# Kernel tuning notes

Measured on AMD Instinct MI355X. Metric: run time of the kernel, lower is better.

The kernel has to match this reference:

```python
import jax, jax.numpy as jnp
import numpy as np

N = 100000      # nodes
E = 1200000     # edges
F = 16          # in_cont_dim
EMB = 8         # emb_dim
H = 64          # hidden_dim
NL = 3          # num_layers
NT = 32         # num_func_types


def setup_inputs() -> dict:
    key = jax.random.key(0)
    ks = jax.random.split(key, 10)
    s = lambda k, sh: jax.random.normal(k, sh, jnp.float32) * 0.05
    inp = {}
    inp["x_cont"] = jax.random.normal(ks[0], (N, F), jnp.float32)
    inp["func_type"] = jax.random.randint(ks[1], (N,), 0, NT)
    inp["edge_index"] = jax.random.randint(ks[2], (2, E), 0, N)
    inp["emb_table"] = s(ks[3], (NT, EMB))
    inp["W_in"] = s(ks[4], (F + EMB, H)); inp["b_in"] = jnp.zeros((H,), jnp.float32)
    inp["W_g"] = s(ks[5], (NL, H, H));    inp["b_g"] = jnp.zeros((NL, H), jnp.float32)
    inp["W_o1"] = s(ks[6], (H, H));       inp["b_o1"] = jnp.zeros((H,), jnp.float32)
    inp["W_o2"] = s(ks[7], (H, 1));       inp["b_o2"] = jnp.zeros((1,), jnp.float32)
    return inp


def _gcn_layer(x, src, dst, deg_isq, W, b):
    # PyG GCNConv: h = x W; out_i = sum_{j->i} d_i^-1/2 d_j^-1/2 h_j + d_i^-1 h_i + b
    h = x @ W                                   # [N, H]
    norm = deg_isq[src] * deg_isq[dst]          # [E]
    agg = jax.ops.segment_sum(norm[:, None] * h[src], dst, num_segments=N)
    agg = agg + (deg_isq * deg_isq)[:, None] * h  # self-loop contribution
    return agg + b


def reference(x_cont, func_type, edge_index, emb_table, W_in, b_in,
              W_g, b_g, W_o1, b_o1, W_o2, b_o2):
    src, dst = edge_index[0], edge_index[1]
    # degree with self loops (weight 1), computed at target nodes as in gcn_norm
    deg = 1.0 + jax.ops.segment_sum(jnp.ones((E,), x_cont.dtype), dst, num_segments=N)
    deg_isq = jax.lax.rsqrt(deg)
    x = jnp.concatenate([x_cont, emb_table[func_type]], axis=-1)  # [N, F+EMB]
    x = jax.nn.relu(x @ W_in + b_in)
    for i in range(NL):
        x = jax.nn.relu(_gcn_layer(x, src, dst, deg_isq, W_g[i], b_g[i]))
        # dropout is identity in eval mode
    h = jax.nn.relu(x @ W_o1 + b_o1)
    return (h @ W_o2 + b_o2)[:, 0]  # [N]
```

## Files before the change

### kernel.cpp

```cpp
#include <hip/hip_runtime.h>

#define HD 64
#define FC 16
#define FEMB 8

__device__ __forceinline__ float bfu(unsigned u) { return __uint_as_float(u); }
__device__ __forceinline__ unsigned short f2bf(float f) {
    unsigned u = __float_as_uint(f);
    return (unsigned short)((u + 0x7fffu + ((u >> 16) & 1u)) >> 16);
}

__global__ void k_count_rank(const int* __restrict__ dst, int* __restrict__ cnt,
                             int* __restrict__ rank, int E) {
    int t = blockIdx.x * blockDim.x + threadIdx.x;
    int base = t * 4;
    if (base + 4 <= E) {
        int4 d = *(const int4*)(dst + base);
        int r0 = atomicAdd(&cnt[d.x], 1);
        int r1 = atomicAdd(&cnt[d.y], 1);
        int r2 = atomicAdd(&cnt[d.z], 1);
        int r3 = atomicAdd(&cnt[d.w], 1);
        *(int4*)(rank + base) = make_int4(r0, r1, r2, r3);
    } else {
        for (int e = base; e < E; e++)
            rank[e] = atomicAdd(&cnt[dst[e]], 1);
    }
}

__global__ void k_scan1(const int* __restrict__ cnt, int* __restrict__ row_part,
                        int* __restrict__ bsum, float* __restrict__ disq, int n) {
    __shared__ int s[256];
    int t = threadIdx.x;
    int i = blockIdx.x * 256 + t;
    int v = (i < n) ? cnt[i] : 0;
    if (i < n) disq[i] = rsqrtf(1.0f + (float)v);
    s[t] = v;
    __syncthreads();
    for (int off = 1; off < 256; off <<= 1) {
        int a = (t >= off) ? s[t - off] : 0;
        __syncthreads();
        s[t] += a;
        __syncthreads();
    }
    if (i < n) row_part[i] = s[t] - v;
    if (t == 255) bsum[blockIdx.x] = s[255];
}

__global__ void k_scan2(int* __restrict__ bsum, int nb) {
    __shared__ int s[1024];
    int t = threadIdx.x;
    int v = (t < nb) ? bsum[t] : 0;
    s[t] = v;
    __syncthreads();
    for (int off = 1; off < 1024; off <<= 1) {
        int a = (t >= off) ? s[t - off] : 0;
        __syncthreads();
        s[t] += a;
        __syncthreads();
    }
    if (t < nb) bsum[t] = s[t] - v;
}

__global__ void k_reorder_input(const int* __restrict__ src, const int* __restrict__ dst,
                                const int* __restrict__ rank, const int* __restrict__ row_part,
                                const int* __restrict__ bsum, int* __restrict__ csr, int E,
                                int nbr,
                                const float* __restrict__ xc, const int* __restrict__ ft,
                                const float* __restrict__ emb, const float* __restrict__ Win,
                                const float* __restrict__ bin, const float* __restrict__ disq,
                                unsigned short* __restrict__ y, int n) {
    int b = blockIdx.x;
    if (b < nbr) {
        int g   = b & 7;
        int bg  = b >> 3;
        int nbg = nbr >> 3;
        int slice = n >> 3;
        int lo = g * slice;
        int hi = (g == 7) ? n : lo + slice;
        int stride = nbg * 256;
        for (int e = bg * 256 + (int)threadIdx.x; e < E; e += stride) {
            int d = dst[e];
            if (d >= lo && d < hi) {
                int pos = row_part[d] + bsum[d >> 8] + rank[e];
                csr[pos] = src[e];
            }
        }
    } else {
        int lane = threadIdx.x & 63;
        int wid  = (((b - nbr) * 256 + (int)threadIdx.x) >> 6);
        if (wid >= n) return;
        float acc = bin[lane];
        const float* xr = xc + (size_t)wid * FC;
#pragma unroll
        for (int k = 0; k < FC; k++)
            acc = fmaf(xr[k], Win[k * HD + lane], acc);
        int t = ft[wid];
        const float* er = emb + (size_t)t * FEMB;
#pragma unroll
        for (int k = 0; k < FEMB; k++)
            acc = fmaf(er[k], Win[(FC + k) * HD + lane], acc);
        y[(size_t)wid * HD + lane] = f2bf(fmaxf(acc, 0.0f) * disq[wid]);
    }
}

__global__ void k_agg(const uint4* __restrict__ y4, const int* __restrict__ csr,
                      const int* __restrict__ row_part, const int* __restrict__ bsum,
                      const int* __restrict__ cnt,
                      const float* __restrict__ disq, float* __restrict__ agg, int n) {
    int lane = threadIdx.x & 63;
    int node = (blockIdx.x * blockDim.x + threadIdx.x) >> 6;
    if (node >= n) return;
    int g = lane >> 3;
    int c = lane & 7;
    int start = row_part[node] + bsum[node >> 8];
    int deg   = cnt[node];
    int end   = start + deg;
    float di  = disq[node];
    float a0 = 0.f, a1 = 0.f, a2 = 0.f, a3 = 0.f;
    float a4 = 0.f, a5 = 0.f, a6 = 0.f, a7 = 0.f;
    for (int j = start; j < end; j += 16) {
        int e0 = j + g;
        bool ok0 = e0 < end;
        int s0 = csr[ok0 ? e0 : j];
        uint4 v0 = y4[(size_t)s0 * 8 + c];
        if (ok0) {
            a0 += bfu(v0.x << 16); a1 += bfu(v0.x & 0xffff0000u);
            a2 += bfu(v0.y << 16); a3 += bfu(v0.y & 0xffff0000u);
            a4 += bfu(v0.z << 16); a5 += bfu(v0.z & 0xffff0000u);
            a6 += bfu(v0.w << 16); a7 += bfu(v0.w & 0xffff0000u);
        }
        if (j + 8 < end) {
            int e1 = j + 8 + g;
            bool ok1 = e1 < end;
            int s1 = csr[ok1 ? e1 : j];
            uint4 v1 = y4[(size_t)s1 * 8 + c];
            if (ok1) {
                a0 += bfu(v1.x << 16); a1 += bfu(v1.x & 0xffff0000u);
                a2 += bfu(v1.y << 16); a3 += bfu(v1.y & 0xffff0000u);
                a4 += bfu(v1.z << 16); a5 += bfu(v1.z & 0xffff0000u);
                a6 += bfu(v1.w << 16); a7 += bfu(v1.w & 0xffff0000u);
            }
        }
    }
#define RED8(off) \
    a0 += __shfl_xor(a0, off); a1 += __shfl_xor(a1, off); \
    a2 += __shfl_xor(a2, off); a3 += __shfl_xor(a3, off); \
    a4 += __shfl_xor(a4, off); a5 += __shfl_xor(a5, off); \
    a6 += __shfl_xor(a6, off); a7 += __shfl_xor(a7, off);
    RED8(8) RED8(16) RED8(32)
#undef RED8
    if (g == 0) {
        uint4 sv = y4[(size_t)node * 8 + c];
        a0 += bfu(sv.x << 16); a1 += bfu(sv.x & 0xffff0000u);
        a2 += bfu(sv.y << 16); a3 += bfu(sv.y & 0xffff0000u);
        a4 += bfu(sv.z << 16); a5 += bfu(sv.z & 0xffff0000u);
        a6 += bfu(sv.w << 16); a7 += bfu(sv.w & 0xffff0000u);
        float4* ap = (float4*)(agg + (size_t)node * HD + c * 8);
        float4 o1 = {di * a0, di * a1, di * a2, di * a3};
        float4 o2 = {di * a4, di * a5, di * a6, di * a7};
        ap[0] = o1;
        ap[1] = o2;
    }
}

__global__ __launch_bounds__(256, 4)
void k_mm(const float* __restrict__ x, const float* __restrict__ W,
          const float* __restrict__ b, const float* __restrict__ disq,
          unsigned short* __restrict__ yo, int n) {
    __shared__ float4 ws4[64][16];
    __shared__ float4 xs4[64][17];
    int tid = threadIdx.x;
    int node0 = blockIdx.x * 64;

    for (int i = tid; i < 1024; i += 256)
        ws4[i >> 4][i & 15] = ((const float4*)W)[i];
    for (int i = tid; i < 1024; i += 256) {
        int nn = i >> 4, k4 = i & 15;
        int row = node0 + nn; if (row >= n) row = n - 1;
        xs4[nn][k4] = ((const float4*)(x + (size_t)row * HD))[k4];
    }
    __syncthreads();

    int tc4 = tid & 15;
    int tn  = (tid >> 4) * 4;
    float4 ac0 = {0,0,0,0}, ac1 = {0,0,0,0}, ac2 = {0,0,0,0}, ac3 = {0,0,0,0};

#pragma unroll 4
    for (int k4 = 0; k4 < 16; k4++) {
        float4 w0 = ws4[k4 * 4 + 0][tc4];
        float4 w1 = ws4[k4 * 4 + 1][tc4];
        float4 w2 = ws4[k4 * 4 + 2][tc4];
        float4 w3 = ws4[k4 * 4 + 3][tc4];
#pragma unroll
        for (int i = 0; i < 4; i++) {
            float4 xv = xs4[tn + i][k4];
            float4* ac = (i == 0) ? &ac0 : (i == 1) ? &ac1 : (i == 2) ? &ac2 : &ac3;
            ac->x = fmaf(xv.x, w0.x, ac->x); ac->y = fmaf(xv.x, w0.y, ac->y);
            ac->z = fmaf(xv.x, w0.z, ac->z); ac->w = fmaf(xv.x, w0.w, ac->w);
            ac->x = fmaf(xv.y, w1.x, ac->x); ac->y = fmaf(xv.y, w1.y, ac->y);
            ac->z = fmaf(xv.y, w1.z, ac->z); ac->w = fmaf(xv.y, w1.w, ac->w);
            ac->x = fmaf(xv.z, w2.x, ac->x); ac->y = fmaf(xv.z, w2.y, ac->y);
            ac->z = fmaf(xv.z, w2.z, ac->z); ac->w = fmaf(xv.z, w2.w, ac->w);
            ac->x = fmaf(xv.w, w3.x, ac->x); ac->y = fmaf(xv.w, w3.y, ac->y);
            ac->z = fmaf(xv.w, w3.z, ac->z); ac->w = fmaf(xv.w, w3.w, ac->w);
        }
    }

    float4 bb = ((const float4*)b)[tc4];
    float4 accs[4] = {ac0, ac1, ac2, ac3};
#pragma unroll
    for (int i = 0; i < 4; i++) {
        int row = node0 + tn + i;
        if (row < n) {
            float dq = disq[row];
            ushort4 o;
            o.x = f2bf(fmaxf(accs[i].x + bb.x, 0.0f) * dq);
            o.y = f2bf(fmaxf(accs[i].y + bb.y, 0.0f) * dq);
            o.z = f2bf(fmaxf(accs[i].z + bb.z, 0.0f) * dq);
            o.w = f2bf(fmaxf(accs[i].w + bb.w, 0.0f) * dq);
            *(ushort4*)(yo + (size_t)row * HD + tc4 * 4) = o;
        }
    }
}

__global__ __launch_bounds__(256, 4)
void k_mm_head(const float* __restrict__ x, const float* __restrict__ W,
               const float* __restrict__ b, const float* __restrict__ W1,
               const float* __restrict__ b1, const float* __restrict__ W2,
               const float* __restrict__ b2, float* __restrict__ out, int n) {
    __shared__ float4 ws4[64][16];
    __shared__ float4 xs4[64][17];
    int tid = threadIdx.x;
    int node0 = blockIdx.x * 64;

    for (int i = tid; i < 1024; i += 256)
        ws4[i >> 4][i & 15] = ((const float4*)W)[i];
    for (int i = tid; i < 1024; i += 256) {
        int nn = i >> 4, k4 = i & 15;
        int row = node0 + nn; if (row >= n) row = n - 1;
        xs4[nn][k4] = ((const float4*)(x + (size_t)row * HD))[k4];
    }
    __syncthreads();

    int tc4 = tid & 15;
    int tn  = (tid >> 4) * 4;

    float4 ac0 = {0,0,0,0}, ac1 = {0,0,0,0}, ac2 = {0,0,0,0}, ac3 = {0,0,0,0};
#pragma unroll 4
    for (int k4 = 0; k4 < 16; k4++) {
        float4 w0 = ws4[k4 * 4 + 0][tc4];
        float4 w1 = ws4[k4 * 4 + 1][tc4];
        float4 w2 = ws4[k4 * 4 + 2][tc4];
        float4 w3 = ws4[k4 * 4 + 3][tc4];
#pragma unroll
        for (int i = 0; i < 4; i++) {
            float4 xv = xs4[tn + i][k4];
            float4* ac = (i == 0) ? &ac0 : (i == 1) ? &ac1 : (i == 2) ? &ac2 : &ac3;
            ac->x = fmaf(xv.x, w0.x, ac->x); ac->y = fmaf(xv.x, w0.y, ac->y);
            ac->z = fmaf(xv.x, w0.z, ac->z); ac->w = fmaf(xv.x, w0.w, ac->w);
            ac->x = fmaf(xv.y, w1.x, ac->x); ac->y = fmaf(xv.y, w1.y, ac->y);
            ac->z = fmaf(xv.y, w1.z, ac->z); ac->w = fmaf(xv.y, w1.w, ac->w);
            ac->x = fmaf(xv.z, w2.x, ac->x); ac->y = fmaf(xv.z, w2.y, ac->y);
            ac->z = fmaf(xv.z, w2.z, ac->z); ac->w = fmaf(xv.z, w2.w, ac->w);
            ac->x = fmaf(xv.w, w3.x, ac->x); ac->y = fmaf(xv.w, w3.y, ac->y);
            ac->z = fmaf(xv.w, w3.z, ac->z); ac->w = fmaf(xv.w, w3.w, ac->w);
        }
    }
    __syncthreads();

    {
        float4 bb = ((const float4*)b)[tc4];
        float4 accs[4] = {ac0, ac1, ac2, ac3};
#pragma unroll
        for (int i = 0; i < 4; i++) {
            float4 o;
            o.x = fmaxf(accs[i].x + bb.x, 0.0f);
            o.y = fmaxf(accs[i].y + bb.y, 0.0f);
            o.z = fmaxf(accs[i].z + bb.z, 0.0f);
            o.w = fmaxf(accs[i].w + bb.w, 0.0f);
            xs4[tn + i][tc4] = o;
        }
    }
    for (int i = tid; i < 1024; i += 256)
        ws4[i >> 4][i & 15] = ((const float4*)W1)[i];
    __syncthreads();

    float4 bc0 = {0,0,0,0}, bc1 = {0,0,0,0}, bc2 = {0,0,0,0}, bc3 = {0,0,0,0};
#pragma unroll 4
    for (int k4 = 0; k4 < 16; k4++) {
        float4 w0 = ws4[k4 * 4 + 0][tc4];
        float4 w1 = ws4[k4 * 4 + 1][tc4];
        float4 w2 = ws4[k4 * 4 + 2][tc4];
        float4 w3 = ws4[k4 * 4 + 3][tc4];
#pragma unroll
        for (int i = 0; i < 4; i++) {
            float4 xv = xs4[tn + i][k4];
            float4* ac = (i == 0) ? &bc0 : (i == 1) ? &bc1 : (i == 2) ? &bc2 : &bc3;
            ac->x = fmaf(xv.x, w0.x, ac->x); ac->y = fmaf(xv.x, w0.y, ac->y);
            ac->z = fmaf(xv.x, w0.z, ac->z); ac->w = fmaf(xv.x, w0.w, ac->w);
            ac->x = fmaf(xv.y, w1.x, ac->x); ac->y = fmaf(xv.y, w1.y, ac->y);
            ac->z = fmaf(xv.y, w1.z, ac->z); ac->w = fmaf(xv.y, w1.w, ac->w);
            ac->x = fmaf(xv.z, w2.x, ac->x); ac->y = fmaf(xv.z, w2.y, ac->y);
            ac->z = fmaf(xv.z, w2.z, ac->z); ac->w = fmaf(xv.z, w2.w, ac->w);
            ac->x = fmaf(xv.w, w3.x, ac->x); ac->y = fmaf(xv.w, w3.y, ac->y);
            ac->z = fmaf(xv.w, w3.z, ac->z); ac->w = fmaf(xv.w, w3.w, ac->w);
        }
    }

    float4 b1v = ((const float4*)b1)[tc4];
    float4 w2v = ((const float4*)W2)[tc4];
    float b2v  = b2[0];
    float4 bcs[4] = {bc0, bc1, bc2, bc3};
#pragma unroll
    for (int i = 0; i < 4; i++) {
        float s = fmaxf(bcs[i].x + b1v.x, 0.0f) * w2v.x
                + fmaxf(bcs[i].y + b1v.y, 0.0f) * w2v.y
                + fmaxf(bcs[i].z + b1v.z, 0.0f) * w2v.z
                + fmaxf(bcs[i].w + b1v.w, 0.0f) * w2v.w;
        s += __shfl_xor(s, 1);
        s += __shfl_xor(s, 2);
        s += __shfl_xor(s, 4);
        s += __shfl_xor(s, 8);
        int row = node0 + tn + i;
        if (tc4 == 0 && row < n) out[row] = s + b2v;
    }
}

extern "C" void kernel_launch(void* const* d_in, const int* in_sizes, int n_in,
                              void* d_out, int out_size, void* d_ws, size_t ws_size,
                              hipStream_t stream) {
    const float* x_cont = (const float*)d_in[0];
    const int*   ftyp   = (const int*)d_in[1];
    const int*   eidx   = (const int*)d_in[2];
    const float* emb    = (const float*)d_in[3];
    const float* W_in   = (const float*)d_in[4];
    const float* b_in   = (const float*)d_in[5];
    const float* W_g    = (const float*)d_in[6];
    const float* b_g    = (const float*)d_in[7];
    const float* W_o1   = (const float*)d_in[8];
    const float* b_o1   = (const float*)d_in[9];
    const float* W_o2   = (const float*)d_in[10];
    const float* b_o2   = (const float*)d_in[11];
    float* out = (float*)d_out;

    const int n = in_sizes[1];
    const int E = in_sizes[2] / 2;
    const int* src = eidx;
    const int* dst = eidx + E;

    char* p = (char*)d_ws;
    auto alloc = [&](size_t bytes) {
        char* r = p;
        p += (bytes + 255) & ~(size_t)255;
        return r;
    };
    int*      cnt      = (int*)  alloc((size_t)n * 4);
    float*    disq     = (float*)alloc((size_t)n * 4);
    int*      row_part = (int*)  alloc((size_t)n * 4);
    int*      bsum     = (int*)  alloc(4096);
    int*      rank     = (int*)  alloc((size_t)E * 4);
    int*      csr      = (int*)  alloc((size_t)E * 4);
    unsigned short* y16 = (unsigned short*)alloc((size_t)n * HD * 2);
    float*    agg      = (float*)alloc((size_t)n * HD * 4);

    hipMemsetAsync(cnt, 0, (size_t)n * 4, stream);

    dim3 blk(256);
    const int nb1   = (n + 255) / 256;
    const int nb_c  = (E / 4 + 255) / 256;
    const int nbr   = 2048;
    const int nb_nw = (n + 3) / 4;
    const int nb_t  = (n + 63) / 64;

    k_count_rank<<<nb_c, blk, 0, stream>>>(dst, cnt, rank, E);
    k_scan1<<<nb1, blk, 0, stream>>>(cnt, row_part, bsum, disq, n);
    k_scan2<<<1, 1024, 0, stream>>>(bsum, nb1);
    k_reorder_input<<<nbr + nb_nw, blk, 0, stream>>>(
        src, dst, rank, row_part, bsum, csr, E, nbr,
        x_cont, ftyp, emb, W_in, b_in, disq, y16, n);

    for (int L = 0; L < 2; L++) {
        k_agg<<<nb_nw, blk, 0, stream>>>((const uint4*)y16, csr, row_part, bsum,
                                         cnt, disq, agg, n);
        k_mm<<<nb_t, blk, 0, stream>>>(agg, W_g + (size_t)L * HD * HD,
                                       b_g + (size_t)L * HD, disq, y16, n);
    }
    k_agg<<<nb_nw, blk, 0, stream>>>((const uint4*)y16, csr, row_part, bsum,
                                     cnt, disq, agg, n);
    k_mm_head<<<nb_t, blk, 0, stream>>>(agg, W_g + (size_t)2 * HD * HD,
                                        b_g + (size_t)2 * HD,
                                        W_o1, b_o1, W_o2, b_o2, out, n);
}
```

Baseline: 324.3 us.

## Replace per-edge rank array with atomic cursors and pack per-node headers

The count pass no longer records a per-edge rank. The CSR fill instead claims slots through atomicAdd on a per-node cursor seeded by a new header kernel. Each node's start, degree and inverse-sqrt degree are packed into one int4 header, so the aggregation kernels do a single 16-byte load instead of four scattered loads. This removes the E-sized rank write and read, at the cost of contended atomics during the fill, an extra small kernel, and a neighbor order within each row that is no longer deterministic.

```diff
diff --git a/kernel.cpp b/kernel.cpp
--- a/kernel.cpp
+++ b/kernel.cpp
@@ -10,21 +10,19 @@
     return (unsigned short)((u + 0x7fffu + ((u >> 16) & 1u)) >> 16);
 }
 
-__global__ void k_count_rank(const int* __restrict__ dst, int* __restrict__ cnt,
-                             int* __restrict__ rank, int E) {
+__global__ void k_count(const int* __restrict__ dst, int* __restrict__ cnt, int E) {
     int t = blockIdx.x * blockDim.x + threadIdx.x;
-    int base = t * 4;
-    if (base + 4 <= E) {
-        int4 d = *(const int4*)(dst + base);
-        int r0 = atomicAdd(&cnt[d.x], 1);
-        int r1 = atomicAdd(&cnt[d.y], 1);
-        int r2 = atomicAdd(&cnt[d.z], 1);
-        int r3 = atomicAdd(&cnt[d.w], 1);
-        *(int4*)(rank + base) = make_int4(r0, r1, r2, r3);
-    } else {
-        for (int e = base; e < E; e++)
-            rank[e] = atomicAdd(&cnt[dst[e]], 1);
-    }
+    int stride = gridDim.x * blockDim.x;
+    int nv = E >> 2;
+    for (int i = t; i < nv; i += stride) {
+        int4 d = ((const int4*)dst)[i];
+        atomicAdd(&cnt[d.x], 1);
+        atomicAdd(&cnt[d.y], 1);
+        atomicAdd(&cnt[d.z], 1);
+        atomicAdd(&cnt[d.w], 1);
+    }
+    for (int i = (nv << 2) + t; i < E; i += stride)
+        atomicAdd(&cnt[dst[i]], 1);
 }
 
 __global__ void k_scan1(const int* __restrict__ cnt, int* __restrict__ row_part,
@@ -61,9 +59,19 @@
     if (t < nb) bsum[t] = s[t] - v;
 }
 
+__global__ void k_hdr(const int* __restrict__ row_part, const int* __restrict__ bsum,
+                      const int* __restrict__ cnt, const float* __restrict__ disq,
+                      int* __restrict__ cursor, int4* __restrict__ hdr, int n) {
+    int stride = gridDim.x * blockDim.x;
+    for (int i = blockIdx.x * blockDim.x + threadIdx.x; i < n; i += stride) {
+        int st = row_part[i] + bsum[i >> 8];
+        cursor[i] = st;
+        hdr[i] = make_int4(st, cnt[i], __float_as_int(disq[i]), 0);
+    }
+}
+
 __global__ void k_reorder_input(const int* __restrict__ src, const int* __restrict__ dst,
-                                const int* __restrict__ rank, const int* __restrict__ row_part,
-                                const int* __restrict__ bsum, int* __restrict__ csr, int E,
+                                int* __restrict__ cursor, int* __restrict__ csr, int E,
                                 int nbr,
                                 const float* __restrict__ xc, const int* __restrict__ ft,
                                 const float* __restrict__ emb, const float* __restrict__ Win,
@@ -81,7 +89,7 @@
         for (int e = bg * 256 + (int)threadIdx.x; e < E; e += stride) {
             int d = dst[e];
             if (d >= lo && d < hi) {
-                int pos = row_part[d] + bsum[d >> 8] + rank[e];
+                int pos = atomicAdd(&cursor[d], 1);
                 csr[pos] = src[e];
             }
         }
@@ -104,18 +112,17 @@
 }
 
 __global__ void k_agg(const uint4* __restrict__ y4, const int* __restrict__ csr,
-                      const int* __restrict__ row_part, const int* __restrict__ bsum,
-                      const int* __restrict__ cnt,
-                      const float* __restrict__ disq, float* __restrict__ agg, int n) {
+                      const int4* __restrict__ hdr,
+                      float* __restrict__ agg, int n) {
     int lane = threadIdx.x & 63;
     int node = (blockIdx.x * blockDim.x + threadIdx.x) >> 6;
     if (node >= n) return;
     int g = lane >> 3;
     int c = lane & 7;
-    int start = row_part[node] + bsum[node >> 8];
-    int deg   = cnt[node];
-    int end   = start + deg;
-    float di  = disq[node];
+    int4 h = hdr[node];
+    int start = h.x;
+    int end   = start + h.y;
+    float di  = __int_as_float(h.z);
     float a0 = 0.f, a1 = 0.f, a2 = 0.f, a3 = 0.f;
     float a4 = 0.f, a5 = 0.f, a6 = 0.f, a7 = 0.f;
     for (int j = start; j < end; j += 16) {
@@ -358,7 +365,8 @@
     float*    disq     = (float*)alloc((size_t)n * 4);
     int*      row_part = (int*)  alloc((size_t)n * 4);
     int*      bsum     = (int*)  alloc(4096);
-    int*      rank     = (int*)  alloc((size_t)E * 4);
+    int*      cursor   = (int*)  alloc((size_t)n * 4);
+    int4*     hdr      = (int4*) alloc((size_t)n * 16);
     int*      csr      = (int*)  alloc((size_t)E * 4);
     unsigned short* y16 = (unsigned short*)alloc((size_t)n * HD * 2);
     float*    agg      = (float*)alloc((size_t)n * HD * 4);
@@ -367,26 +375,24 @@
 
     dim3 blk(256);
     const int nb1   = (n + 255) / 256;
-    const int nb_c  = (E / 4 + 255) / 256;
     const int nbr   = 2048;
     const int nb_nw = (n + 3) / 4;
     const int nb_t  = (n + 63) / 64;
 
-    k_count_rank<<<nb_c, blk, 0, stream>>>(dst, cnt, rank, E);
+    k_count<<<1024, blk, 0, stream>>>(dst, cnt, E);
     k_scan1<<<nb1, blk, 0, stream>>>(cnt, row_part, bsum, disq, n);
     k_scan2<<<1, 1024, 0, stream>>>(bsum, nb1);
+    k_hdr<<<512, blk, 0, stream>>>(row_part, bsum, cnt, disq, cursor, hdr, n);
     k_reorder_input<<<nbr + nb_nw, blk, 0, stream>>>(
-        src, dst, rank, row_part, bsum, csr, E, nbr,
+        src, dst, cursor, csr, E, nbr,
         x_cont, ftyp, emb, W_in, b_in, disq, y16, n);
 
     for (int L = 0; L < 2; L++) {
-        k_agg<<<nb_nw, blk, 0, stream>>>((const uint4*)y16, csr, row_part, bsum,
-                                         cnt, disq, agg, n);
+        k_agg<<<nb_nw, blk, 0, stream>>>((const uint4*)y16, csr, hdr, agg, n);
         k_mm<<<nb_t, blk, 0, stream>>>(agg, W_g + (size_t)L * HD * HD,
                                        b_g + (size_t)L * HD, disq, y16, n);
     }
-    k_agg<<<nb_nw, blk, 0, stream>>>((const uint4*)y16, csr, row_part, bsum,
-                                     cnt, disq, agg, n);
+    k_agg<<<nb_nw, blk, 0, stream>>>((const uint4*)y16, csr, hdr, agg, n);
     k_mm_head<<<nb_t, blk, 0, stream>>>(agg, W_g + (size_t)2 * HD * HD,
                                         b_g + (size_t)2 * HD,
                                         W_o1, b_o1, W_o2, b_o2, out, n);
```

After: 345.7 us. +6.6%, slower.
